# Kernel optimization log

Hardware: AMD Instinct MI355X
Metric: run time of the kernel (lower is better)

Reference implementation:

```python
import jax, jax.numpy as jnp
import numpy as np

H = 1024

def gru_step(x, h, W_ih, W_hh, b_ih, b_hh):
    # torch.nn.GRUCell math; gate order r, z, n
    gi = x @ W_ih.T + b_ih            # [N, 3H]
    gh = h @ W_hh.T + b_hh            # [N, 3H]
    i_r, i_z, i_n = jnp.split(gi, 3, axis=-1)
    h_r, h_z, h_n = jnp.split(gh, 3, axis=-1)
    r = jax.nn.sigmoid(i_r + h_r)
    z = jax.nn.sigmoid(i_z + h_z)
    n = jnp.tanh(i_n + r * h_n)
    return (1.0 - z) * n + z * h


def setup_inputs() -> dict:
    key = jax.random.key(0)
    ks = jax.random.split(key, 12)
    V, Nr, Na = 256, 4096, 4096
    s = 1.0 / np.sqrt(H)
    return {
        'state': jax.random.normal(ks[0], (1, H), jnp.float32),
        'rel_tokens': jax.random.randint(ks[1], (Nr, 3), 0, V, jnp.int32),
        'attr_tokens': jax.random.randint(ks[2], (Na, 2), 0, V, jnp.int32),
        'table': jax.random.normal(ks[3], (V, H), jnp.float32),
        'W_emb': jax.random.normal(ks[4], (H, H), jnp.float32) * s,
        'b_emb': jnp.zeros((H,), jnp.float32),
        'W_ih': jax.random.normal(ks[5], (3 * H, H), jnp.float32) * s,
        'W_hh': jax.random.normal(ks[6], (3 * H, H), jnp.float32) * s,
        'b_ih': jnp.zeros((3 * H,), jnp.float32),
        'b_hh': jnp.zeros((3 * H,), jnp.float32),
        'W1': jax.random.normal(ks[7], (H, H), jnp.float32) * s,
        'b1': jnp.zeros((H,), jnp.float32),
        'W2': jax.random.normal(ks[8], (H, H), jnp.float32) * s,
        'b2': jnp.zeros((H,), jnp.float32),
        'W3': jax.random.normal(ks[9], (1, H), jnp.float32) * s,
        'b3': jnp.zeros((1,), jnp.float32),
        'eps': jax.random.uniform(ks[10], (1,), jnp.float32) * 0.1,
    }


def reference(state, rel_tokens, attr_tokens, table, W_emb, b_emb,
              W_ih, W_hh, b_ih, b_hh, W1, b1, W2, b2, W3, b3, eps):
    Nr, Na = rel_tokens.shape[0], attr_tokens.shape[0]
    # per-clause token embeddings passed through embedding_layer (Linear)
    rel_e = jnp.einsum('nte,he->nth', table[rel_tokens], W_emb) + b_emb   # [Nr,3,H]
    att_e = jnp.einsum('nte,he->nth', table[attr_tokens], W_emb) + b_emb  # [Na,2,H]

    # relation clauses: 3 chained GRU steps from global state
    h = jnp.broadcast_to(state, (Nr, H))
    for t in range(3):
        h = gru_step(rel_e[:, t], h, W_ih, W_hh, b_ih, b_hh)
    rel_h = h
    # attribute clauses: 2 chained GRU steps from global state
    h = jnp.broadcast_to(state, (Na, H))
    for t in range(2):
        h = gru_step(att_e[:, t], h, W_ih, W_hh, b_ih, b_hh)
    attr_h = h

    clause = jnp.concatenate([rel_h, attr_h], axis=0)          # [N, H]
    x = jax.nn.relu(clause @ W1.T + b1)
    x = jax.nn.relu(x @ W2.T + b2)
    logits = (x @ W3.T + b3).reshape(1, -1)                    # [1, N]
    probs = jax.nn.softmax(logits, axis=1)                     # softmax over clauses
    n = jnp.float32(probs.shape[1])
    probs = probs * (1.0 - eps[0]) + eps[0] / n                # eps smoothing
    return probs
```

## Files before the change

kernel.cpp:

```cpp
#include <hip/hip_runtime.h>
#include <math.h>

#define H 1024
#define H3 3072
#define NVOC 256

typedef __attribute__((ext_vector_type(8))) short bf16x8;
typedef __attribute__((ext_vector_type(4))) float f32x4;

__device__ __forceinline__ float sigf(float x) { return 1.0f / (1.0f + expf(-x)); }

__device__ __forceinline__ unsigned short f2bf(float f) {
    unsigned int u = __float_as_uint(f);
    u = (u + 0x7fffu + ((u >> 16) & 1u)) >> 16;
    return (unsigned short)u;
}
__device__ __forceinline__ float bf2f(unsigned short u) {
    return __uint_as_float(((unsigned int)u) << 16);
}

template<bool RELU, int OUT_MODE>
__global__ __launch_bounds__(256)
void gemm_bf16(const unsigned short* __restrict__ A, const unsigned short* __restrict__ W,
               const float* __restrict__ bias, void* __restrict__ C,
               int N, int K, int gx, int Kc,
               const float* __restrict__ w3, float* __restrict__ logits)
{
    __shared__ unsigned short As[4][128 * 32];
    __shared__ unsigned short Ws[4][128 * 32];
    const int tid = threadIdx.x;
    const int wid = tid >> 6, lane = tid & 63;

    const int nwg = gridDim.x;
    const int cpx = nwg >> 3;
    const int bid = blockIdx.x;
    const int swz = (bid & 7) * cpx + (bid >> 3);
    const int bm = (swz / gx) * 128;
    const int bn = (swz % gx) * 128;
    const int k_base = blockIdx.y * Kc;
    const int nt = Kc >> 5;

    const int wm = (wid >> 1) * 64, wn = (wid & 1) * 64;
    const int fr = lane & 15;
    const int fq = lane >> 4;
    const int perm = fq ^ (fr & 3);

    f32x4 acc[4][4];
#pragma unroll
    for (int i = 0; i < 4; i++)
#pragma unroll
        for (int j = 0; j < 4; j++) acc[i][j] = (f32x4){0.f, 0.f, 0.f, 0.f};

    const int srow = tid >> 2;
    const int schunk = (tid & 3) ^ (srow & 3);
    const unsigned short* aS = A + (size_t)(bm + srow) * K + k_base + schunk * 8;
    const unsigned short* wS = W + (size_t)(bn + srow) * K + k_base + schunk * 8;
    const size_t rstep = (size_t)64 * K;

    auto stage = [&](int b, int t) {
        const unsigned short* a0 = aS + t * 32;
        const unsigned short* w0 = wS + t * 32;
        __builtin_amdgcn_global_load_lds(
            (const __attribute__((address_space(1))) void*)a0,
            (__attribute__((address_space(3))) void*)(&As[b][wid * 512]), 16, 0, 0);
        __builtin_amdgcn_global_load_lds(
            (const __attribute__((address_space(1))) void*)(a0 + rstep),
            (__attribute__((address_space(3))) void*)(&As[b][2048 + wid * 512]), 16, 0, 0);
        __builtin_amdgcn_global_load_lds(
            (const __attribute__((address_space(1))) void*)w0,
            (__attribute__((address_space(3))) void*)(&Ws[b][wid * 512]), 16, 0, 0);
        __builtin_amdgcn_global_load_lds(
            (const __attribute__((address_space(1))) void*)(w0 + rstep),
            (__attribute__((address_space(3))) void*)(&Ws[b][2048 + wid * 512]), 16, 0, 0);
    };

    stage(0, 0);
    if (nt > 1) stage(1, 1);
    if (nt > 2) stage(2, 2);

    for (int t = 0; t < nt; ++t) {
        if (t + 2 < nt)      asm volatile("s_waitcnt vmcnt(8)" ::: "memory");
        else if (t + 1 < nt) asm volatile("s_waitcnt vmcnt(4)" ::: "memory");
        else                 asm volatile("s_waitcnt vmcnt(0)" ::: "memory");
        __builtin_amdgcn_s_barrier();
        __builtin_amdgcn_sched_barrier(0);
        if (t + 3 < nt) stage((t + 3) & 3, t + 3);

        const unsigned short* as = &As[t & 3][0];
        const unsigned short* ws = &Ws[t & 3][0];
        bf16x8 a[4], b[4];
#pragma unroll
        for (int m = 0; m < 4; m++)
            a[m] = *reinterpret_cast<const bf16x8*>(as + (wm + m * 16 + fr) * 32 + perm * 8);
#pragma unroll
        for (int n = 0; n < 4; n++)
            b[n] = *reinterpret_cast<const bf16x8*>(ws + (wn + n * 16 + fr) * 32 + perm * 8);
        __builtin_amdgcn_s_setprio(1);
#pragma unroll
        for (int m = 0; m < 4; m++)
#pragma unroll
            for (int n = 0; n < 4; n++)
                acc[m][n] = __builtin_amdgcn_mfma_f32_16x16x32_bf16(a[m], b[n], acc[m][n], 0, 0, 0);
        __builtin_amdgcn_s_setprio(0);
    }

    if (OUT_MODE == 2) {
        float rs[4][4];
#pragma unroll
        for (int m = 0; m < 4; m++)
#pragma unroll
            for (int j = 0; j < 4; j++) rs[m][j] = 0.f;
#pragma unroll
        for (int n = 0; n < 4; n++) {
            const int col = bn + wn + n * 16 + fr;
            const float bv = bias[col];
            const float wv = w3[col];
#pragma unroll
            for (int m = 0; m < 4; m++)
#pragma unroll
                for (int j = 0; j < 4; j++) {
                    float v = acc[m][n][j] + bv;
                    if (RELU) v = fmaxf(v, 0.f);
                    rs[m][j] = fmaf(v, wv, rs[m][j]);
                }
        }
#pragma unroll
        for (int m = 0; m < 4; m++)
#pragma unroll
            for (int j = 0; j < 4; j++) {
                float s = rs[m][j];
                s += __shfl_xor(s, 1); s += __shfl_xor(s, 2);
                s += __shfl_xor(s, 4); s += __shfl_xor(s, 8);
                if (fr == 0) atomicAdd(logits + bm + wm + m * 16 + fq * 4 + j, s);
            }
    } else if (OUT_MODE == 3) {
        float* Cf = (float*)C;
#pragma unroll
        for (int m = 0; m < 4; m++)
#pragma unroll
            for (int n = 0; n < 4; n++) {
                const int col = bn + wn + n * 16 + fr;
#pragma unroll
                for (int j = 0; j < 4; j++) {
                    const int row = bm + wm + m * 16 + fq * 4 + j;
                    atomicAdd(Cf + (size_t)row * N + col, acc[m][n][j]);
                }
            }
    } else {
#pragma unroll
        for (int m = 0; m < 4; m++) {
#pragma unroll
            for (int n = 0; n < 4; n++) {
                const int col = bn + wn + n * 16 + fr;
                const float bv = bias[col];
#pragma unroll
                for (int j = 0; j < 4; j++) {
                    const int row = bm + wm + m * 16 + fq * 4 + j;
                    float v = acc[m][n][j] + bv;
                    if (RELU) v = fmaxf(v, 0.f);
                    if (OUT_MODE == 1)
                        ((unsigned short*)C)[(size_t)row * N + col] = f2bf(v);
                    else
                        ((float*)C)[(size_t)row * N + col] = v;
                }
            }
        }
    }
}

__global__ void cvt_all(const float* __restrict__ W_hh, const float* __restrict__ W_ih,
                        const float* __restrict__ W1, const float* __restrict__ W2,
                        const float* __restrict__ W_emb, const float* __restrict__ table,
                        unsigned short* __restrict__ W_hhb, unsigned short* __restrict__ W_ihb,
                        unsigned short* __restrict__ W1b, unsigned short* __restrict__ W2b,
                        unsigned short* __restrict__ W_embb, unsigned short* __restrict__ tableb)
{
    const int C1 = H3 * H, C2 = H * H, C3 = NVOC * H;
    int off = (blockIdx.x * blockDim.x + threadIdx.x) * 4;
    const float* src; unsigned short* dst;
    if (off < C1)               { src = W_hh;  dst = W_hhb; }
    else if ((off -= C1) < C1)  { src = W_ih;  dst = W_ihb; }
    else if ((off -= C1) < C2)  { src = W1;    dst = W1b; }
    else if ((off -= C2) < C2)  { src = W2;    dst = W2b; }
    else if ((off -= C2) < C2)  { src = W_emb; dst = W_embb; }
    else if ((off -= C2) < C3)  { src = table; dst = tableb; }
    else return;
    float4 v = *reinterpret_cast<const float4*>(src + off);
    ushort4 o;
    o.x = f2bf(v.x); o.y = f2bf(v.y); o.z = f2bf(v.z); o.w = f2bf(v.w);
    *reinterpret_cast<ushort4*>(dst + off) = o;
}

__global__ void prefill(const float* __restrict__ b_emb, const float* __restrict__ b_ih,
                        const float* __restrict__ b_hh,
                        float* __restrict__ emb32, float* __restrict__ Gi,
                        float* __restrict__ gh1, float* __restrict__ logits, int Ntot)
{
    const int E = NVOC * H, G = NVOC * H3;
    int i = blockIdx.x * blockDim.x + threadIdx.x;
    if (i < E)                { emb32[i] = b_emb[i & (H - 1)]; return; }
    if ((i -= E) < G)         { Gi[i] = b_ih[i % H3]; return; }
    if ((i -= G) < G)         { gh1[i] = b_hh[i % H3]; return; }
    if ((i -= G) < Ntot)      logits[i] = 0.f;
}

__global__ void cvt_emb(const float* __restrict__ in, unsigned short* __restrict__ out)
{
    int i = (blockIdx.x * blockDim.x + threadIdx.x) * 4;
    float4 v = *reinterpret_cast<const float4*>(in + i);
    ushort4 o;
    o.x = f2bf(v.x); o.y = f2bf(v.y); o.z = f2bf(v.z); o.w = f2bf(v.w);
    *reinterpret_cast<ushort4*>(out + i) = o;
}

__global__ void gemv_bf16w(const float* __restrict__ x, const unsigned short* __restrict__ Wm,
                           const float* __restrict__ bias, float* __restrict__ out,
                           int N, int K)
{
    int wid = threadIdx.x >> 6;
    int lane = threadIdx.x & 63;
    int n = blockIdx.x * (blockDim.x >> 6) + wid;
    if (n >= N) return;
    const unsigned short* wr = Wm + (size_t)n * K;
    float s = 0.f;
    for (int p = 0; p < K; p += 256) {
        float4 xv = *reinterpret_cast<const float4*>(x + p + lane * 4);
        ushort4 wv = *reinterpret_cast<const ushort4*>(wr + p + lane * 4);
        s = fmaf(xv.x, bf2f(wv.x), s); s = fmaf(xv.y, bf2f(wv.y), s);
        s = fmaf(xv.z, bf2f(wv.z), s); s = fmaf(xv.w, bf2f(wv.w), s);
    }
#pragma unroll
    for (int off = 32; off; off >>= 1) s += __shfl_down(s, off);
    if (lane == 0) out[n] = s + (bias ? bias[n] : 0.f);
}

__global__ void h1_combine(const float* __restrict__ Gi, const float* __restrict__ gh0,
                           const float* __restrict__ state, float* __restrict__ h1,
                           unsigned short* __restrict__ h1b)
{
    int idx = blockIdx.x * blockDim.x + threadIdx.x;
    int v = idx >> 10, h = idx & (H - 1);
    const float* g = Gi + (size_t)v * H3;
    float r = sigf(g[h] + gh0[h]);
    float z = sigf(g[H + h] + gh0[H + h]);
    float n = tanhf(fmaf(r, gh0[2 * H + h], g[2 * H + h]));
    float v2 = (1.f - z) * n + z * state[h];
    h1[idx] = v2;
    h1b[idx] = f2bf(v2);
}

__global__ void step2_both(const int* __restrict__ rel, const int* __restrict__ attr, int Nr,
                           const float* __restrict__ Gi, const float* __restrict__ gh1,
                           const float* __restrict__ h1,
                           unsigned short* __restrict__ h2b, unsigned short* __restrict__ attr_out)
{
    int idx = blockIdx.x * blockDim.x + threadIdx.x;
    int row = idx >> 10, h = idx & (H - 1);
    int t0, t1, orow = row;
    unsigned short* dst;
    if (row < Nr) { t0 = rel[row * 3 + 0]; t1 = rel[row * 3 + 1]; dst = h2b; }
    else { orow = row - Nr; t0 = attr[orow * 2 + 0]; t1 = attr[orow * 2 + 1]; dst = attr_out; }
    const float* g = Gi + (size_t)t1 * H3;
    const float* gh = gh1 + (size_t)t0 * H3;
    float r = sigf(g[h] + gh[h]);
    float z = sigf(g[H + h] + gh[H + h]);
    float n = tanhf(fmaf(r, gh[2 * H + h], g[2 * H + h]));
    float v = (1.f - z) * n + z * h1[(size_t)t0 * H + h];
    dst[(size_t)orow * H + h] = f2bf(v);
}

__global__ void step3_rel(const int* __restrict__ toks,
                          const float* __restrict__ Gi, const unsigned short* __restrict__ gh2b,
                          const unsigned short* __restrict__ h2b, unsigned short* __restrict__ outb)
{
    int idx = blockIdx.x * blockDim.x + threadIdx.x;
    int row = idx >> 10, h = idx & (H - 1);
    int t2 = toks[row * 3 + 2];
    const float* g = Gi + (size_t)t2 * H3;
    const unsigned short* gh = gh2b + (size_t)row * H3;
    float r = sigf(g[h] + bf2f(gh[h]));
    float z = sigf(g[H + h] + bf2f(gh[H + h]));
    float n = tanhf(fmaf(r, bf2f(gh[2 * H + h]), g[2 * H + h]));
    outb[idx] = f2bf((1.f - z) * n + z * bf2f(h2b[idx]));
}

__global__ void softmax_eps(const float* __restrict__ logits, const float* __restrict__ epsp,
                            float* __restrict__ out, int N)
{
    __shared__ float smax[16], ssum[16];
    int tid = threadIdx.x;
    int nw = blockDim.x >> 6;
    float m = -INFINITY;
    for (int i = tid; i < N; i += blockDim.x) m = fmaxf(m, logits[i]);
#pragma unroll
    for (int off = 32; off; off >>= 1) m = fmaxf(m, __shfl_down(m, off));
    if ((tid & 63) == 0) smax[tid >> 6] = m;
    __syncthreads();
    float M = smax[0];
    for (int i = 1; i < nw; i++) M = fmaxf(M, smax[i]);
    float s = 0.f;
    for (int i = tid; i < N; i += blockDim.x) s += expf(logits[i] - M);
#pragma unroll
    for (int off = 32; off; off >>= 1) s += __shfl_down(s, off);
    if ((tid & 63) == 0) ssum[tid >> 6] = s;
    __syncthreads();
    float S = 0.f;
    for (int i = 0; i < nw; i++) S += ssum[i];
    float e = epsp[0];
    float mul = (1.f - e) / S;
    float add = e / (float)N;
    for (int i = tid; i < N; i += blockDim.x) out[i] = expf(logits[i] - M) * mul + add;
}

extern "C" void kernel_launch(void* const* d_in, const int* in_sizes, int n_in,
                              void* d_out, int out_size, void* d_ws, size_t ws_size,
                              hipStream_t stream)
{
    const float* state       = (const float*)d_in[0];
    const int*   rel_tokens  = (const int*)d_in[1];
    const int*   attr_tokens = (const int*)d_in[2];
    const float* table       = (const float*)d_in[3];
    const float* W_emb       = (const float*)d_in[4];
    const float* b_emb       = (const float*)d_in[5];
    const float* W_ih        = (const float*)d_in[6];
    const float* W_hh        = (const float*)d_in[7];
    const float* b_ih        = (const float*)d_in[8];
    const float* b_hh        = (const float*)d_in[9];
    const float* W1          = (const float*)d_in[10];
    const float* b1          = (const float*)d_in[11];
    const float* W2          = (const float*)d_in[12];
    const float* b2          = (const float*)d_in[13];
    const float* W3          = (const float*)d_in[14];
    const float* eps         = (const float*)d_in[16];

    const int Nr = in_sizes[1] / 3;
    const int Na = in_sizes[2] / 2;
    const int Ntot = Nr + Na;

    float* ws     = (float*)d_ws;
    float* Gi     = ws;
    float* gh0    = Gi + NVOC * H3;
    float* h1     = gh0 + H3;
    float* gh1    = h1 + NVOC * H;
    float* emb32  = gh1 + NVOC * H3;
    float* logits = emb32 + NVOC * H;
    unsigned short* W_hhb   = (unsigned short*)(logits + Ntot);
    unsigned short* W_ihb   = W_hhb + (size_t)H3 * H;
    unsigned short* W1b     = W_ihb + (size_t)H3 * H;
    unsigned short* W2b     = W1b + (size_t)H * H;
    unsigned short* W_embb  = W2b + (size_t)H * H;
    unsigned short* tableb  = W_embb + (size_t)H * H;
    unsigned short* embb    = tableb + (size_t)NVOC * H;
    unsigned short* h1b     = embb + (size_t)NVOC * H;
    unsigned short* h2b     = h1b + (size_t)NVOC * H;
    unsigned short* gh2b    = h2b + (size_t)Nr * H;
    unsigned short* clauseb = gh2b + (size_t)Nr * H3;
    unsigned short* x1b     = clauseb + (size_t)Ntot * H;

    {
        const int total = 2 * H3 * H + 3 * H * H + NVOC * H;
        cvt_all<<<(total / 4 + 255) / 256, 256, 0, stream>>>(
            W_hh, W_ih, W1, W2, W_emb, table,
            W_hhb, W_ihb, W1b, W2b, W_embb, tableb);
        const int pf = NVOC * H + 2 * NVOC * H3 + Ntot;
        prefill<<<(pf + 255) / 256, 256, 0, stream>>>(b_emb, b_ih, b_hh,
                                                      emb32, Gi, gh1, logits, Ntot);
    }

    gemm_bf16<false, 3><<<dim3((H / 128) * (NVOC / 128), 4), 256, 0, stream>>>(
        tableb, W_embb, nullptr, emb32, H, H, H / 128, H / 4, nullptr, nullptr);
    cvt_emb<<<NVOC * H / 4 / 256, 256, 0, stream>>>(emb32, embb);
    gemm_bf16<false, 3><<<dim3((H3 / 128) * (NVOC / 128), 4), 256, 0, stream>>>(
        embb, W_ihb, nullptr, Gi, H3, H, H3 / 128, H / 4, nullptr, nullptr);
    gemv_bf16w<<<H3 / 4, 256, 0, stream>>>(state, W_hhb, b_hh, gh0, H3, H);
    h1_combine<<<NVOC * H / 256, 256, 0, stream>>>(Gi, gh0, state, h1, h1b);
    gemm_bf16<false, 3><<<dim3((H3 / 128) * (NVOC / 128), 4), 256, 0, stream>>>(
        h1b, W_hhb, nullptr, gh1, H3, H, H3 / 128, H / 4, nullptr, nullptr);
    step2_both<<<Ntot * (H / 256), 256, 0, stream>>>(rel_tokens, attr_tokens, Nr,
                                                     Gi, gh1, h1, h2b,
                                                     clauseb + (size_t)Nr * H);
    gemm_bf16<false, 1><<<dim3((H3 / 128) * (Nr / 128), 1), 256, 0, stream>>>(
        h2b, W_hhb, b_hh, gh2b, H3, H, H3 / 128, H, nullptr, nullptr);
    step3_rel<<<Nr * (H / 256), 256, 0, stream>>>(rel_tokens, Gi, gh2b, h2b, clauseb);
    gemm_bf16<true, 1><<<dim3((H / 128) * (Ntot / 128), 1), 256, 0, stream>>>(
        clauseb, W1b, b1, x1b, H, H, H / 128, H, nullptr, nullptr);
    gemm_bf16<true, 2><<<dim3((H / 128) * (Ntot / 128), 1), 256, 0, stream>>>(
        x1b, W2b, b2, nullptr, H, H, H / 128, H, W3, logits);
    softmax_eps<<<1, 1024, 0, stream>>>(logits, eps, (float*)d_out, Ntot);
}
```

Before: 319.1 us.

## Add 256x256-tile 8-wave GEMM with double-buffered direct-to-LDS loads for large GEMMs

Adds a new bf16 MFMA GEMM kernel with 256x256 output tiles, 512 threads, and a 128 KB double-buffered LDS ring filled by global_load_lds. The stage loads are interleaved with MFMA sub-blocks under explicit vmcnt waits and barriers. It replaces the 128x128 kernel for the step-3 hidden GEMM and the two MLP GEMMs, including the fused W3 logit reduction, to raise arithmetic intensity and overlap loads with compute. The trade-off is fewer workgroups per GEMM (e.g. 192 or 128 tiles), which may leave CUs idle, plus heavier register and LDS use.

```diff
diff --git a/kernel.cpp b/kernel.cpp
--- a/kernel.cpp
+++ b/kernel.cpp
@@ -17,6 +17,188 @@
 }
 __device__ __forceinline__ float bf2f(unsigned short u) {
     return __uint_as_float(((unsigned int)u) << 16);
+}
+
+#define MM256(MH, AV, BV)                                                          \
+    __builtin_amdgcn_s_setprio(1);                                                 \
+    _Pragma("unroll")                                                              \
+    for (int m_ = 0; m_ < 4; ++m_)                                                 \
+        _Pragma("unroll")                                                          \
+        for (int n_ = 0; n_ < 4; ++n_)                                             \
+            acc[(MH) * 4 + m_][n_] = __builtin_amdgcn_mfma_f32_16x16x32_bf16(      \
+                AV[m_], BV[n_], acc[(MH) * 4 + m_][n_], 0, 0, 0);                  \
+    __builtin_amdgcn_s_setprio(0);
+
+#define RDA256(BUF, KQ, MH)                                                        \
+    _Pragma("unroll")                                                              \
+    for (int m_ = 0; m_ < 4; ++m_)                                                 \
+        a[m_] = *reinterpret_cast<const bf16x8*>(                                  \
+            ldsb + (BUF) * 65536 + ((KQ) * 2 + (MH)) * 8192 + m_ * 1024 + aoff);
+
+#define RDB256(BUF, KQ, DST)                                                       \
+    _Pragma("unroll")                                                              \
+    for (int n_ = 0; n_ < 4; ++n_)                                                 \
+        DST[n_] = *reinterpret_cast<const bf16x8*>(                                \
+            ldsb + (BUF) * 65536 + (KQ) * 16384 + n_ * 1024 + boff);
+
+#define BAR256() __builtin_amdgcn_s_barrier()
+
+template<bool RELU, int OUT_MODE>
+__global__ __launch_bounds__(512, 2)
+void gemm256(const unsigned short* __restrict__ A, const unsigned short* __restrict__ W,
+             const float* __restrict__ bias, void* __restrict__ C,
+             int N, int K, int gx,
+             const float* __restrict__ w3, float* __restrict__ logits)
+{
+    __shared__ unsigned short lds[65536];
+    char* ldsb = (char*)lds;
+    const int tid = threadIdx.x;
+    const int wid = tid >> 6, lane = tid & 63;
+
+    const int nwg = gridDim.x;
+    const int cpx = nwg >> 3;
+    const int bid = blockIdx.x;
+    const int swz = (bid & 7) * cpx + (bid >> 3);
+    const int bm = (swz / gx) * 256;
+    const int bn = (swz % gx) * 256;
+
+    const int g = wid >> 2;
+    const int wn = (wid & 3) * 64;
+    const int fr = lane & 15, fq = lane >> 4;
+
+    const int aoff = (g * 64 + fr) * 64 + ((fq ^ (fr & 3)) * 16);
+    const int boff = (wn + fr) * 64 + ((fq ^ (fr & 3)) * 16) + 32768;
+
+    const int srow = tid >> 2;
+    const int scol = ((tid & 3) ^ (srow & 3)) * 8;
+    const int arow0 = ((srow >> 6) << 7) + (srow & 63);
+
+    auto stageA = [&](int t, int mh) {
+        const int buf = t & 1;
+        const unsigned short* src = A + (size_t)(bm + arow0 + mh * 64) * K + t * 64 + scol;
+#pragma unroll
+        for (int kh = 0; kh < 2; ++kh) {
+            char* dst = ldsb + buf * 65536 + (kh * 2 + mh) * 8192 + wid * 1024;
+            __builtin_amdgcn_global_load_lds(
+                (const __attribute__((address_space(1))) void*)(src + kh * 32),
+                (__attribute__((address_space(3))) void*)dst, 16, 0, 0);
+        }
+    };
+    auto stageB = [&](int t, int kh) {
+        const int buf = t & 1;
+        const unsigned short* src = W + (size_t)(bn + srow) * K + t * 64 + kh * 32 + scol;
+#pragma unroll
+        for (int j = 0; j < 2; ++j) {
+            char* dst = ldsb + buf * 65536 + 32768 + kh * 16384 + j * 8192 + wid * 1024;
+            __builtin_amdgcn_global_load_lds(
+                (const __attribute__((address_space(1))) void*)(src + (size_t)j * 128 * K),
+                (__attribute__((address_space(3))) void*)dst, 16, 0, 0);
+        }
+    };
+
+    f32x4 acc[8][4];
+#pragma unroll
+    for (int i = 0; i < 8; i++)
+#pragma unroll
+        for (int j = 0; j < 4; j++) acc[i][j] = (f32x4){0.f, 0.f, 0.f, 0.f};
+    bf16x8 a[4], b0[4], b1[4];
+
+    const int nt = K >> 6;
+    const int nIter = nt >> 1;
+
+    stageB(0, 0); stageA(0, 0); stageB(0, 1); stageA(0, 1);
+    stageB(1, 0); stageA(1, 0); stageB(1, 1);
+    asm volatile("s_waitcnt vmcnt(6)" ::: "memory");
+    __builtin_amdgcn_sched_barrier(0);
+    BAR256();
+
+    for (int it = 0; it < nIter; ++it) {
+        const int t0 = 2 * it;
+        const bool full = (it + 1 < nIter);
+        RDB256(0, 0, b0); RDA256(0, 0, 0);
+        stageA(t0 + 1, 1);
+        MM256(0, a, b0); BAR256();
+        RDB256(0, 1, b1); RDA256(0, 1, 0);
+        if (full) stageB(t0 + 2, 0);
+        MM256(0, a, b1); BAR256();
+        RDA256(0, 0, 1);
+        if (full) stageA(t0 + 2, 0);
+        MM256(1, a, b0); BAR256();
+        RDA256(0, 1, 1);
+        if (full) stageB(t0 + 2, 1);
+        MM256(1, a, b1);
+        if (full) { asm volatile("s_waitcnt vmcnt(6)" ::: "memory"); }
+        else      { asm volatile("s_waitcnt vmcnt(0)" ::: "memory"); }
+        __builtin_amdgcn_sched_barrier(0);
+        BAR256();
+        RDB256(1, 0, b0); RDA256(1, 0, 0);
+        if (full) stageA(t0 + 2, 1);
+        MM256(0, a, b0); BAR256();
+        RDB256(1, 1, b1); RDA256(1, 1, 0);
+        if (full) stageB(t0 + 3, 0);
+        MM256(0, a, b1); BAR256();
+        RDA256(1, 0, 1);
+        if (full) stageA(t0 + 3, 0);
+        MM256(1, a, b0); BAR256();
+        RDA256(1, 1, 1);
+        if (full) stageB(t0 + 3, 1);
+        MM256(1, a, b1);
+        if (full) {
+            asm volatile("s_waitcnt vmcnt(6)" ::: "memory");
+            __builtin_amdgcn_sched_barrier(0);
+        }
+        BAR256();
+    }
+
+    if (OUT_MODE == 2) {
+        float rs[8][4];
+#pragma unroll
+        for (int m = 0; m < 8; m++)
+#pragma unroll
+            for (int j = 0; j < 4; j++) rs[m][j] = 0.f;
+#pragma unroll
+        for (int n = 0; n < 4; n++) {
+            const int col = bn + wn + n * 16 + fr;
+            const float bv = bias[col];
+            const float wv = w3[col];
+#pragma unroll
+            for (int m = 0; m < 8; m++)
+#pragma unroll
+                for (int j = 0; j < 4; j++) {
+                    float v = acc[m][n][j] + bv;
+                    if (RELU) v = fmaxf(v, 0.f);
+                    rs[m][j] = fmaf(v, wv, rs[m][j]);
+                }
+        }
+#pragma unroll
+        for (int m = 0; m < 8; m++)
+#pragma unroll
+            for (int j = 0; j < 4; j++) {
+                float s = rs[m][j];
+                s += __shfl_xor(s, 1); s += __shfl_xor(s, 2);
+                s += __shfl_xor(s, 4); s += __shfl_xor(s, 8);
+                if (fr == 0) {
+                    const int row = bm + g * 128 + (m >> 2) * 64 + (m & 3) * 16 + fq * 4 + j;
+                    atomicAdd(logits + row, s);
+                }
+            }
+    } else {
+#pragma unroll
+        for (int m = 0; m < 8; m++) {
+#pragma unroll
+            for (int n = 0; n < 4; n++) {
+                const int col = bn + wn + n * 16 + fr;
+                const float bv = bias[col];
+#pragma unroll
+                for (int j = 0; j < 4; j++) {
+                    const int row = bm + g * 128 + (m >> 2) * 64 + (m & 3) * 16 + fq * 4 + j;
+                    float v = acc[m][n][j] + bv;
+                    if (RELU) v = fmaxf(v, 0.f);
+                    ((unsigned short*)C)[(size_t)row * N + col] = f2bf(v);
+                }
+            }
+        }
+    }
 }
 
 template<bool RELU, int OUT_MODE>
@@ -104,36 +286,7 @@
         __builtin_amdgcn_s_setprio(0);
     }
 
-    if (OUT_MODE == 2) {
-        float rs[4][4];
-#pragma unroll
-        for (int m = 0; m < 4; m++)
-#pragma unroll
-            for (int j = 0; j < 4; j++) rs[m][j] = 0.f;
-#pragma unroll
-        for (int n = 0; n < 4; n++) {
-            const int col = bn + wn + n * 16 + fr;
-            const float bv = bias[col];
-            const float wv = w3[col];
-#pragma unroll
-            for (int m = 0; m < 4; m++)
-#pragma unroll
-                for (int j = 0; j < 4; j++) {
-                    float v = acc[m][n][j] + bv;
-                    if (RELU) v = fmaxf(v, 0.f);
-                    rs[m][j] = fmaf(v, wv, rs[m][j]);
-                }
-        }
-#pragma unroll
-        for (int m = 0; m < 4; m++)
-#pragma unroll
-            for (int j = 0; j < 4; j++) {
-                float s = rs[m][j];
-                s += __shfl_xor(s, 1); s += __shfl_xor(s, 2);
-                s += __shfl_xor(s, 4); s += __shfl_xor(s, 8);
-                if (fr == 0) atomicAdd(logits + bm + wm + m * 16 + fq * 4 + j, s);
-            }
-    } else if (OUT_MODE == 3) {
+    if (OUT_MODE == 3) {
         float* Cf = (float*)C;
 #pragma unroll
         for (int m = 0; m < 4; m++)
@@ -379,12 +532,12 @@
     step2_both<<<Ntot * (H / 256), 256, 0, stream>>>(rel_tokens, attr_tokens, Nr,
                                                      Gi, gh1, h1, h2b,
                                                      clauseb + (size_t)Nr * H);
-    gemm_bf16<false, 1><<<dim3((H3 / 128) * (Nr / 128), 1), 256, 0, stream>>>(
-        h2b, W_hhb, b_hh, gh2b, H3, H, H3 / 128, H, nullptr, nullptr);
+    gemm256<false, 1><<<(Nr / 256) * (H3 / 256), 512, 0, stream>>>(
+        h2b, W_hhb, b_hh, gh2b, H3, H, H3 / 256, nullptr, nullptr);
     step3_rel<<<Nr * (H / 256), 256, 0, stream>>>(rel_tokens, Gi, gh2b, h2b, clauseb);
-    gemm_bf16<true, 1><<<dim3((H / 128) * (Ntot / 128), 1), 256, 0, stream>>>(
-        clauseb, W1b, b1, x1b, H, H, H / 128, H, nullptr, nullptr);
-    gemm_bf16<true, 2><<<dim3((H / 128) * (Ntot / 128), 1), 256, 0, stream>>>(
-        x1b, W2b, b2, nullptr, H, H, H / 128, H, W3, logits);
+    gemm256<true, 1><<<(Ntot / 256) * (H / 256), 512, 0, stream>>>(
+        clauseb, W1b, b1, x1b, H, H, H / 256, nullptr, nullptr);
+    gemm256<true, 2><<<(Ntot / 256) * (H / 256), 512, 0, stream>>>(
+        x1b, W2b, b2, nullptr, H, H, H / 256, W3, logits);
     softmax_eps<<<1, 1024, 0, stream>>>(logits, eps, (float*)d_out, Ntot);
 }
```

After: 311.7 us. 1.02x faster.
